# Optimization experiments

Hardware: AMD Instinct MI355X
Metric: run time of the kernel (lower is better)

The kernel has to match this reference:

```python
import jax, jax.numpy as jnp
import numpy as np

B, S, D, H, HS, FF, L, V = 8, 512, 512, 8, 64, 2048, 6, 1024
EPS = 1e-5


def _layer_norm(x, g, b):
    m = jnp.mean(x, axis=-1, keepdims=True)
    v = jnp.var(x, axis=-1, keepdims=True)
    return (x - m) * jax.lax.rsqrt(v + EPS) * g + b


def _pos_encoding(seq_len, d, dtype):
    # Faithful to source: exponent uses 2*i/seq_len (x.shape[seq_dim]), not d_model.
    pos = jnp.arange(seq_len, dtype=dtype)[:, None]
    i = jnp.arange(d)
    pe = pos / (10000.0 ** (2.0 * i.astype(dtype) / seq_len))
    return jnp.where(i % 2 == 0, jnp.sin(pe), jnp.cos(pe))


def setup_inputs() -> dict:
    key = jax.random.key(0)
    ks = jax.random.split(key, 16)
    tok_ids = jax.random.randint(ks[0], (B, S), 0, V)
    tokens = jax.nn.one_hot(tok_ids, V, dtype=jnp.float32)
    std = 0.02
    return {
        "tokens": tokens,
        "token_embeddings": jax.random.normal(ks[1], (V, D), jnp.float32),
        "qkv_w": jax.random.normal(ks[2], (L, H, D, 3 * HS), jnp.float32) * std,
        "qkv_b": jnp.zeros((L, H, 3 * HS), jnp.float32),
        "out_w": jax.random.normal(ks[3], (L, D, D), jnp.float32) * std,
        "out_b": jnp.zeros((L, D), jnp.float32),
        "w1": jax.random.normal(ks[4], (L, D, FF), jnp.float32) * std,
        "b1": jnp.zeros((L, FF), jnp.float32),
        "w2": jax.random.normal(ks[5], (L, FF, D), jnp.float32) * std,
        "b2": jnp.zeros((L, D), jnp.float32),
        "ln1_g": jnp.ones((L, D), jnp.float32),
        "ln1_b": jnp.zeros((L, D), jnp.float32),
        "ln2_g": jnp.ones((L, D), jnp.float32),
        "ln2_b": jnp.zeros((L, D), jnp.float32),
    }


def _forward(tokens, token_embeddings, qkv_w, qkv_b, out_w, out_b,
             w1, b1, w2, b2, ln1_g, ln1_b, ln2_g, ln2_b):
    dt = tokens.dtype
    x = tokens @ (token_embeddings * (D ** 0.5))          # [B,S,D]
    x = x + _pos_encoding(S, D, dt)
    # Multiplicative causal mask (faithful to source: -1e6 strictly above diag, 0 elsewhere)
    mask = jnp.triu(jnp.full((S, S), -1e6, dt), k=1)
    scale = 1.0 / (HS ** 0.5)

    def block(x, p):
        (qw, qb, ow, ob, w1_, b1_, w2_, b2_, g1, be1, g2, be2) = p
        qkv = jnp.einsum('bsd,hdk->bhsk', x, qw) + qb[None, :, None, :]
        q, k, v = jnp.split(qkv, 3, axis=-1)              # each [B,H,S,HS]
        logits = jnp.einsum('bhsk,bhtk->bhst', q, k)      # [B,H,S,S]
        attn = jax.nn.softmax(logits * mask * scale, axis=-1)
        o = jnp.einsum('bhst,bhtk->bhsk', attn, v)
        o = o.transpose(0, 2, 1, 3).reshape(x.shape[0], S, D)  # concat heads
        o = o @ ow + ob
        x = _layer_norm(x + o, g1, be1)
        h = jax.nn.relu(x @ w1_ + b1_) @ w2_ + b2_
        x = _layer_norm(x + h, g2, be2)
        return x, None

    params = (qkv_w, qkv_b, out_w, out_b, w1, b1, w2, b2, ln1_g, ln1_b, ln2_g, ln2_b)
    x, _ = jax.lax.scan(block, x, params)
    return x @ token_embeddings.T                          # [B,S,V]


def reference(tokens, token_embeddings, qkv_w, qkv_b, out_w, out_b,
              w1, b1, w2, b2, ln1_g, ln1_b, ln2_g, ln2_b):
    return _forward(tokens, token_embeddings, qkv_w, qkv_b, out_w, out_b,
                    w1, b1, w2, b2, ln1_g, ln1_b, ln2_g, ln2_b)
```

## Files before the change

kernel.cpp:

```cpp
#include <hip/hip_runtime.h>
#include <math.h>

#define BB 8
#define SS 512
#define DD 512
#define HH 8
#define HSD 64
#define FFD 2048
#define LL 6
#define VV 1024
#define NROWS (BB*SS)
#define EPS 1e-5f

__global__ __launch_bounds__(256)
void embed_kernel(const float* __restrict__ tokens,
                  const float* __restrict__ emb,
                  float* __restrict__ x)
{
    const int n = blockIdx.x;
    const int s = n & (SS - 1);
    const int t = threadIdx.x;
    __shared__ int sidx;
    #pragma unroll
    for (int r = 0; r < 4; ++r) {
        int v = t + 256 * r;
        if (tokens[(long)n * VV + v] > 0.5f) sidx = v;
    }
    __syncthreads();
    const int idx = sidx;
    const float sq = 22.62741699796952f;
    #pragma unroll
    for (int r = 0; r < 2; ++r) {
        int d = t + 256 * r;
        float e = emb[(long)idx * DD + d] * sq;
        float expo  = (2.0f * (float)d) / 512.0f;
        float denom = powf(10000.0f, expo);
        float val   = (float)s / denom;
        float pe = ((d & 1) == 0) ? sinf(val) : cosf(val);
        x[(long)n * DD + d] = e + pe;
    }
}

__device__ __forceinline__ void gll16(const float* g, float* l)
{
    __builtin_amdgcn_global_load_lds(
        (const __attribute__((address_space(1))) void*)g,
        (__attribute__((address_space(3))) void*)l, 16, 0, 0);
}

template<int TNB, bool BT, bool QKVB, bool BIAS, bool RELU, bool RES, int SPLITK>
__global__ __launch_bounds__(256)
void gemm_t(const float* __restrict__ A, const float* __restrict__ B,
            const float* __restrict__ bias, const float* __restrict__ res,
            float* __restrict__ C,
            int M, int N, int K, int lda, int ldb, int ldc)
{
    constexpr int NW   = TNB / 16;
    constexpr int BSTR = BT ? (TNB + 4) : TNB;
    constexpr int CPW  = TNB / 32;
    constexpr int CLOG = (TNB == 128) ? 7 : 6;
    const int t  = threadIdx.x;
    const int w  = t >> 6;
    const int ln = t & 63;
    const int bm = blockIdx.y * 128;
    const int bn = blockIdx.x * TNB;
    __shared__ float As[32][132];
    __shared__ __align__(16) float Bs[32][BSTR];
    const int tx = t & 15;
    const int ty = t >> 4;
    float acc[8][NW] = {};

    const int kspan = K / SPLITK;
    const int kbase = (SPLITK > 1) ? blockIdx.z * kspan : 0;

    for (int k0 = kbase; k0 < kbase + kspan; k0 += 32) {
        if (QKVB || !BT) {
            #pragma unroll
            for (int p = 0; p < CPW; ++p) {
                int ch = w * CPW + p;
                int fo = ch * 256 + ln * 4;
                int r  = fo >> CLOG;
                int c  = fo & (TNB - 1);
                const float* src;
                if (QKVB) {
                    int col = bn + c;
                    int hh = (int)((unsigned)col / 192u);
                    int j  = col - hh * 192;
                    src = B + (long)hh * (DD * 192) + (long)(k0 + r) * 192 + j;
                } else {
                    src = B + (long)(k0 + r) * ldb + bn + c;
                }
                gll16(src, &Bs[0][0] + ch * 256);
            }
        } else {
            #pragma unroll
            for (int p = 0; p < TNB / 32; ++p) {
                int q = t + 256 * p;
                int r = q >> 3, kc = (q & 7) * 4;
                float4 b4 = *(const float4*)(B + (long)(bn + r) * ldb + k0 + kc);
                Bs[kc + 0][r] = b4.x; Bs[kc + 1][r] = b4.y;
                Bs[kc + 2][r] = b4.z; Bs[kc + 3][r] = b4.w;
            }
        }
        #pragma unroll
        for (int p = 0; p < 4; ++p) {
            int q = t + 256 * p;
            int r = q >> 3, kc = (q & 7) * 4;
            float4 a4 = *(const float4*)(A + (long)(bm + r) * lda + k0 + kc);
            As[kc + 0][r] = a4.x; As[kc + 1][r] = a4.y;
            As[kc + 2][r] = a4.z; As[kc + 3][r] = a4.w;
        }
        __syncthreads();
        #pragma unroll
        for (int kk = 0; kk < 32; ++kk) {
            float a[8], bv[NW];
            *(float4*)&a[0] = *(const float4*)&As[kk][ty * 8];
            *(float4*)&a[4] = *(const float4*)&As[kk][ty * 8 + 4];
            #pragma unroll
            for (int g = 0; g < NW / 4; ++g)
                *(float4*)&bv[g * 4] = *(const float4*)&Bs[kk][tx * NW + g * 4];
            #pragma unroll
            for (int ii = 0; ii < 8; ++ii)
                #pragma unroll
                for (int jj = 0; jj < NW; ++jj)
                    acc[ii][jj] += a[ii] * bv[jj];
        }
        __syncthreads();
    }

    float* Cp = (SPLITK > 1) ? (C + (long)blockIdx.z * ((long)M * ldc)) : C;
    #pragma unroll
    for (int ii = 0; ii < 8; ++ii) {
        int r = bm + ty * 8 + ii;
        #pragma unroll
        for (int jj = 0; jj < NW; ++jj) {
            int c = bn + tx * NW + jj;
            float v = acc[ii][jj];
            if (BIAS) v += bias[c];
            if (RELU) v = fmaxf(v, 0.0f);
            if (RES)  v += res[(long)r * ldc + c];
            Cp[(long)r * ldc + c] = v;
        }
    }
}

__global__ __launch_bounds__(256)
void attn_kernel(const float* __restrict__ qkv, float* __restrict__ oc)
{
    const int wid = blockIdx.x + (SS / 16) * (blockIdx.y + HH * blockIdx.z);
    const int wl  = (wid & 7) * 256 + (wid >> 3);
    const int b   = wl >> 8;
    const int h   = (wl >> 5) & 7;
    const int i0  = (wl & 31) * 16;

    const int t  = threadIdx.x;
    const int w  = t >> 6;
    const int ln = t & 63;

    __shared__ __align__(16) float Qs[16][64];
    __shared__ __align__(16) float KV[2][64 * 64];
    __shared__ __align__(16) float Zb[16][512];

    const float* __restrict__ base = qkv + (long)b * SS * 1536 + (long)h * 192;

    const int rB = ln >> 4;
    const int g0 = ln & 15;
    const int gx = g0 ^ rB;

    const int kt_start = i0 >> 6;

    gll16(base + (long)(i0 + 4 * w + rB) * 1536 + g0 * 4, &Qs[4 * w][0]);
    #pragma unroll
    for (int p = 0; p < 4; ++p) {
        int q = 4 * w + p;
        int r = 4 * q + rB;
        int g = (gx ^ (p << 2)) << 2;
        gll16(base + (long)(kt_start * 64 + r) * 1536 + 64 + g, &KV[0][q * 256]);
    }
    __syncthreads();

    for (int kt = 0; kt < kt_start; ++kt) {
        #pragma unroll
        for (int c = 0; c < 4; ++c)
            Zb[4 * w + c][kt * 64 + ln] = 0.0f;
    }

    for (int kt = kt_start; kt < 8; ++kt) {
        const int cur = (kt - kt_start) & 1;
        float* nb = &KV[cur ^ 1][0];
        if (kt < 7) {
            const int j0n = (kt + 1) * 64;
            #pragma unroll
            for (int p = 0; p < 4; ++p) {
                int q = 4 * w + p;
                int r = 4 * q + rB;
                int g = (gx ^ (p << 2)) << 2;
                gll16(base + (long)(j0n + r) * 1536 + 64 + g, nb + q * 256);
            }
        } else {
            #pragma unroll
            for (int p = 0; p < 4; ++p) {
                int q = 4 * w + p;
                int r = 4 * q + rB;
                gll16(base + (long)r * 1536 + 128 + g0 * 4, nb + q * 256);
            }
        }

        const float* cb = &KV[cur][0];
        float4 kreg[16];
        #pragma unroll
        for (int kk = 0; kk < 16; ++kk)
            kreg[kk] = *(const float4*)(cb + ln * 64 + ((kk ^ g0) << 2));

        const int j0 = kt * 64;
        #pragma unroll
        for (int c = 0; c < 4; ++c) {
            const int i = 4 * w + c;
            const float4* q4 = (const float4*)&Qs[i][0];
            float dot = 0.0f;
            #pragma unroll
            for (int kk = 0; kk < 16; ++kk) {
                float4 kv = kreg[kk];
                float4 qq = q4[kk];
                dot += qq.x * kv.x + qq.y * kv.y + qq.z * kv.z + qq.w * kv.w;
            }
            const int gi = i0 + i, gj = j0 + ln;
            Zb[i][j0 + ln] = (gj <= gi) ? 0.0f : (dot * -1.0e6f) * 0.125f;
        }
        __syncthreads();
    }

    #pragma unroll
    for (int c = 0; c < 4; ++c) {
        const int i = 4 * w + c;
        float p[8];
        float mx = -3.4e38f;
        #pragma unroll
        for (int r = 0; r < 8; ++r) { p[r] = Zb[i][r * 64 + ln]; mx = fmaxf(mx, p[r]); }
        #pragma unroll
        for (int o = 32; o >= 1; o >>= 1) mx = fmaxf(mx, __shfl_xor(mx, o));
        float sum = 0.0f;
        #pragma unroll
        for (int r = 0; r < 8; ++r) { p[r] = expf(p[r] - mx); sum += p[r]; }
        #pragma unroll
        for (int o = 32; o >= 1; o >>= 1) sum += __shfl_xor(sum, o);
        const float inv = 1.0f / sum;
        #pragma unroll
        for (int r = 0; r < 8; ++r) Zb[i][r * 64 + ln] = p[r] * inv;
    }

    float oA[4] = {0.0f, 0.0f, 0.0f, 0.0f};
    for (int kt = 0; kt < 8; ++kt) {
        const int cur = (kt + kt_start) & 1;
        if (kt < 7) {
            float* nb = &KV[cur ^ 1][0];
            const int j0n = (kt + 1) * 64;
            #pragma unroll
            for (int p = 0; p < 4; ++p) {
                int q = 4 * w + p;
                int r = 4 * q + rB;
                gll16(base + (long)(j0n + r) * 1536 + 128 + g0 * 4, nb + q * 256);
            }
        }

        const float* cb = &KV[cur][0];
        float vreg[64];
        #pragma unroll
        for (int kk = 0; kk < 64; ++kk) vreg[kk] = cb[kk * 64 + ln];

        const int j0 = kt * 64;
        #pragma unroll
        for (int c = 0; c < 4; ++c) {
            const int i = 4 * w + c;
            const float4* pr = (const float4*)&Zb[i][j0];
            float acc = oA[c];
            #pragma unroll
            for (int kk = 0; kk < 16; ++kk) {
                float4 pv = pr[kk];
                acc += pv.x * vreg[kk * 4 + 0];
                acc += pv.y * vreg[kk * 4 + 1];
                acc += pv.z * vreg[kk * 4 + 2];
                acc += pv.w * vreg[kk * 4 + 3];
            }
            oA[c] = acc;
        }
        if (kt < 7) __syncthreads();
    }

    #pragma unroll
    for (int c = 0; c < 4; ++c) {
        const int gi = i0 + 4 * w + c;
        oc[(long)(b * SS + gi) * DD + h * HSD + ln] = oA[c];
    }
}

__device__ __forceinline__ float blk_sum(float v, float* sb)
{
    #pragma unroll
    for (int m = 32; m >= 1; m >>= 1) v += __shfl_xor(v, m);
    if ((threadIdx.x & 63) == 0) sb[threadIdx.x >> 6] = v;
    __syncthreads();
    v = sb[0] + sb[1] + sb[2] + sb[3];
    __syncthreads();
    return v;
}

template<int NP>
__global__ __launch_bounds__(256)
void ln_fuse_kernel(const float* __restrict__ P, const float* __restrict__ bias,
                    const float* __restrict__ res,
                    const float* __restrict__ g, const float* __restrict__ bb,
                    float* __restrict__ out)
{
    __shared__ float sb[4];
    const int n = blockIdx.x;
    const int t = threadIdx.x;
    float v0 = P[(long)n * DD + t];
    float v1 = P[(long)n * DD + t + 256];
    #pragma unroll
    for (int p = 1; p < NP; ++p) {
        v0 += P[(long)p * NROWS * DD + (long)n * DD + t];
        v1 += P[(long)p * NROWS * DD + (long)n * DD + t + 256];
    }
    v0 += bias[t];       v1 += bias[t + 256];
    v0 += res[(long)n * DD + t];
    v1 += res[(long)n * DD + t + 256];

    float total = blk_sum(v0 + v1, sb);
    float mean = total * (1.0f / 512.0f);
    float d0 = v0 - mean, d1 = v1 - mean;
    float ss = blk_sum(d0 * d0 + d1 * d1, sb);
    float var = ss * (1.0f / 512.0f);
    float inv = 1.0f / sqrtf(var + EPS);
    out[(long)n * DD + t]       = d0 * inv * g[t]       + bb[t];
    out[(long)n * DD + t + 256] = d1 * inv * g[t + 256] + bb[t + 256];
}

extern "C" void kernel_launch(void* const* d_in, const int* in_sizes, int n_in,
                              void* d_out, int out_size, void* d_ws, size_t ws_size,
                              hipStream_t stream)
{
    const float* tokens = (const float*)d_in[0];
    const float* emb    = (const float*)d_in[1];
    const float* qkv_w  = (const float*)d_in[2];
    const float* qkv_b  = (const float*)d_in[3];
    const float* out_w  = (const float*)d_in[4];
    const float* out_b  = (const float*)d_in[5];
    const float* w1     = (const float*)d_in[6];
    const float* b1     = (const float*)d_in[7];
    const float* w2     = (const float*)d_in[8];
    const float* b2     = (const float*)d_in[9];
    const float* ln1_g  = (const float*)d_in[10];
    const float* ln1_b  = (const float*)d_in[11];
    const float* ln2_g  = (const float*)d_in[12];
    const float* ln2_b  = (const float*)d_in[13];
    float* out = (float*)d_out;

    float* ws  = (float*)d_ws;
    float* x   = ws;
    float* y   = x  + (long)NROWS * DD;
    float* oc  = y  + (long)NROWS * DD;
    float* big = oc + (long)NROWS * DD;
    float* opP  = big;
    float* ffP  = y;

    embed_kernel<<<NROWS, 256, 0, stream>>>(tokens, emb, x);

    for (int l = 0; l < LL; ++l) {
        const float* qw  = qkv_w + (long)l * HH * DD * 192;
        const float* qb  = qkv_b + (long)l * HH * 192;
        const float* ow  = out_w + (long)l * DD * DD;
        const float* ob  = out_b + (long)l * DD;
        const float* w1l = w1 + (long)l * DD * FFD;
        const float* b1l = b1 + (long)l * FFD;
        const float* w2l = w2 + (long)l * FFD * DD;
        const float* b2l = b2 + (long)l * DD;

        gemm_t<64, false, true, true, false, false, 1><<<dim3(24, 32), 256, 0, stream>>>(
            x, qw, qb, nullptr, big, NROWS, 1536, DD, DD, 192, 1536);

        attn_kernel<<<dim3(SS / 16, HH, BB), 256, 0, stream>>>(big, oc);

        gemm_t<64, false, false, false, false, false, 2><<<dim3(8, 32, 2), 256, 0, stream>>>(
            oc, ow, nullptr, nullptr, opP, NROWS, DD, DD, DD, DD, DD);

        ln_fuse_kernel<2><<<NROWS, 256, 0, stream>>>(
            opP, ob, x, ln1_g + (long)l * DD, ln1_b + (long)l * DD, x);

        gemm_t<128, false, false, true, true, false, 1><<<dim3(16, 32), 256, 0, stream>>>(
            x, w1l, b1l, nullptr, big, NROWS, FFD, DD, DD, FFD, FFD);

        gemm_t<64, false, false, false, false, false, 2><<<dim3(8, 32, 2), 256, 0, stream>>>(
            big, w2l, nullptr, nullptr, ffP, NROWS, DD, FFD, FFD, DD, DD);

        ln_fuse_kernel<2><<<NROWS, 256, 0, stream>>>(
            ffP, b2l, x, ln2_g + (long)l * DD, ln2_b + (long)l * DD, x);
    }

    gemm_t<64, true, false, false, false, false, 1><<<dim3(16, 32), 256, 0, stream>>>(
        x, emb, nullptr, nullptr, out, NROWS, VV, DD, DD, DD, VV);
}
```

Baseline: 3.134 ms.

## Use 128-thread blocks with 8x8 per-thread tiles for TNB=64 GEMMs

Adds a threads-per-block template parameter to the SIMT GEMM so the 128x64 tile configurations run with 128 threads, each computing an 8x8 output micro-tile instead of 8x4. The load loops and thread-to-tile mapping are generalized to match. The aim is more register-level reuse per LDS read, which cuts shared-memory traffic per FMA, at the cost of more registers per thread and fewer waves per block for hiding latency.

```diff
diff --git a/kernel.cpp b/kernel.cpp
--- a/kernel.cpp
+++ b/kernel.cpp
@@ -48,17 +48,22 @@
         (__attribute__((address_space(3))) void*)l, 16, 0, 0);
 }
 
-template<int TNB, bool BT, bool QKVB, bool BIAS, bool RELU, bool RES, int SPLITK>
-__global__ __launch_bounds__(256)
+template<int TPB, int TNB, bool BT, bool QKVB, bool BIAS, bool RELU, bool RES, int SPLITK>
+__global__ __launch_bounds__(TPB)
 void gemm_t(const float* __restrict__ A, const float* __restrict__ B,
             const float* __restrict__ bias, const float* __restrict__ res,
             float* __restrict__ C,
             int M, int N, int K, int lda, int ldb, int ldc)
 {
-    constexpr int NW   = TNB / 16;
+    constexpr int NW   = (TPB == 128) ? 8 : (TNB / 16);
+    constexpr int TCOL = TNB / NW;
+    constexpr int TSH  = (TCOL == 16) ? 4 : 3;
     constexpr int BSTR = BT ? (TNB + 4) : TNB;
-    constexpr int CPW  = TNB / 32;
+    constexpr int NCH  = TNB / 8;
+    constexpr int CPW  = NCH / (TPB / 64);
     constexpr int CLOG = (TNB == 128) ? 7 : 6;
+    constexpr int AF4  = 1024 / TPB;
+    constexpr int BF4  = 8 * TNB / TPB;
     const int t  = threadIdx.x;
     const int w  = t >> 6;
     const int ln = t & 63;
@@ -66,8 +71,8 @@
     const int bn = blockIdx.x * TNB;
     __shared__ float As[32][132];
     __shared__ __align__(16) float Bs[32][BSTR];
-    const int tx = t & 15;
-    const int ty = t >> 4;
+    const int tx = t & (TCOL - 1);
+    const int ty = t >> TSH;
     float acc[8][NW] = {};
 
     const int kspan = K / SPLITK;
@@ -94,8 +99,8 @@
             }
         } else {
             #pragma unroll
-            for (int p = 0; p < TNB / 32; ++p) {
-                int q = t + 256 * p;
+            for (int p = 0; p < BF4; ++p) {
+                int q = t + TPB * p;
                 int r = q >> 3, kc = (q & 7) * 4;
                 float4 b4 = *(const float4*)(B + (long)(bn + r) * ldb + k0 + kc);
                 Bs[kc + 0][r] = b4.x; Bs[kc + 1][r] = b4.y;
@@ -103,8 +108,8 @@
             }
         }
         #pragma unroll
-        for (int p = 0; p < 4; ++p) {
-            int q = t + 256 * p;
+        for (int p = 0; p < AF4; ++p) {
+            int q = t + TPB * p;
             int r = q >> 3, kc = (q & 7) * 4;
             float4 a4 = *(const float4*)(A + (long)(bm + r) * lda + k0 + kc);
             As[kc + 0][r] = a4.x; As[kc + 1][r] = a4.y;
@@ -376,27 +381,27 @@
         const float* w2l = w2 + (long)l * FFD * DD;
         const float* b2l = b2 + (long)l * DD;
 
-        gemm_t<64, false, true, true, false, false, 1><<<dim3(24, 32), 256, 0, stream>>>(
+        gemm_t<128, 64, false, true, true, false, false, 1><<<dim3(24, 32), 128, 0, stream>>>(
             x, qw, qb, nullptr, big, NROWS, 1536, DD, DD, 192, 1536);
 
         attn_kernel<<<dim3(SS / 16, HH, BB), 256, 0, stream>>>(big, oc);
 
-        gemm_t<64, false, false, false, false, false, 2><<<dim3(8, 32, 2), 256, 0, stream>>>(
+        gemm_t<128, 64, false, false, false, false, false, 2><<<dim3(8, 32, 2), 128, 0, stream>>>(
             oc, ow, nullptr, nullptr, opP, NROWS, DD, DD, DD, DD, DD);
 
         ln_fuse_kernel<2><<<NROWS, 256, 0, stream>>>(
             opP, ob, x, ln1_g + (long)l * DD, ln1_b + (long)l * DD, x);
 
-        gemm_t<128, false, false, true, true, false, 1><<<dim3(16, 32), 256, 0, stream>>>(
+        gemm_t<256, 128, false, false, true, true, false, 1><<<dim3(16, 32), 256, 0, stream>>>(
             x, w1l, b1l, nullptr, big, NROWS, FFD, DD, DD, FFD, FFD);
 
-        gemm_t<64, false, false, false, false, false, 2><<<dim3(8, 32, 2), 256, 0, stream>>>(
+        gemm_t<128, 64, false, false, false, false, false, 2><<<dim3(8, 32, 2), 128, 0, stream>>>(
             big, w2l, nullptr, nullptr, ffP, NROWS, DD, FFD, FFD, DD, DD);
 
         ln_fuse_kernel<2><<<NROWS, 256, 0, stream>>>(
             ffP, b2l, x, ln2_g + (long)l * DD, ln2_b + (long)l * DD, x);
     }
 
-    gemm_t<64, true, false, false, false, false, 1><<<dim3(16, 32), 256, 0, stream>>>(
+    gemm_t<128, 64, true, false, false, false, false, 1><<<dim3(16, 32), 128, 0, stream>>>(
         x, emb, nullptr, nullptr, out, NROWS, VV, DD, DD, DD, VV);
 }
```

Measured after the change: 3.681 ms. +17.4%, slower.
